# Kernel optimization log

Measured on AMD Instinct MI355X. Metric: run time of the kernel, lower is better.

The kernel has to match this reference:

```python
import jax, jax.numpy as jnp
import numpy as np

N_NODES = 50000
N_EDGES = 800000
BATCH = 4
D = 64


def setup_inputs() -> dict:
    key = jax.random.key(0)
    ks = jax.random.split(key, 8)
    state = jax.random.normal(ks[0], (BATCH, N_NODES, D), dtype=jnp.float32)
    edge_row = jax.random.randint(ks[1], (N_EDGES,), 0, N_NODES, dtype=jnp.int32)
    edge_col = jax.random.randint(ks[2], (N_EDGES,), 0, N_NODES, dtype=jnp.int32)
    edge_weight = jax.random.uniform(ks[3], (N_EDGES,), dtype=jnp.float32)
    stdv = 1.0 / np.sqrt(D)
    W1 = jax.random.uniform(ks[4], (D, D), minval=-stdv, maxval=stdv, dtype=jnp.float32)
    b1 = jnp.zeros((D,), dtype=jnp.float32)
    W2 = jax.random.uniform(ks[5], (D, D), minval=-stdv, maxval=stdv, dtype=jnp.float32)
    b2 = jnp.zeros((D,), dtype=jnp.float32)
    w_out = jax.random.normal(ks[6], (D,), dtype=jnp.float32) * stdv
    return {"state": state, "edge_row": edge_row, "edge_col": edge_col,
            "edge_weight": edge_weight, "W1": W1, "b1": b1, "W2": W2,
            "b2": b2, "w_out": w_out}


def _gcn_layer(x, W, bias, edge_row, edge_col, edge_weight, n, b):
    # x: [n, b, d_in] -> support [n, b, d_out]
    support = jnp.einsum('nbk,kp->nbp', x, W) + bias
    flat = support.reshape(n, -1)  # [n, b*d_out]
    # sparse spmm: out[i] = sum_{e: row_e=i} w_e * flat[col_e]
    msgs = edge_weight[:, None] * flat[edge_col]  # [E, b*d_out]
    out = jax.ops.segment_sum(msgs, edge_row, num_segments=n)
    return jax.nn.relu(out.reshape(n, b, -1))


def reference(state, edge_row, edge_col, edge_weight, W1, b1, W2, b2, w_out):
    b, n, _ = state.shape
    x = jnp.transpose(state, (1, 0, 2))  # [n, b, d]
    for W, bias in ((W1, b1), (W2, b2)):
        x = _gcn_layer(x, W, bias, edge_row, edge_col, edge_weight, n, b)
    # actor head: Linear(d,1,bias=False), squeeze, transpose -> [b, n]
    logits = jnp.einsum('nbd,d->nb', x, w_out)
    return logits.T
```

## Files before the change

### kernel.cpp

```cpp
#include <hip/hip_runtime.h>


typedef _Float16 fp16_t;
typedef _Float16 h4 __attribute__((ext_vector_type(4)));
typedef _Float16 h8 __attribute__((ext_vector_type(8)));
typedef float    f4 __attribute__((ext_vector_type(4)));
typedef unsigned long long ull;

#define CAP   64
#define RPB   256
#define BCAP  4608
#define CHK   3200
#define LROW  264
#define S1Q   (127.f / 4.f)
#define S1D   (4.f / 127.f)

__global__ __launch_bounds__(64) void prepW_k(const float* __restrict__ W,
                                              const float* __restrict__ bias,
                                              fp16_t* __restrict__ wf,
                                              float* __restrict__ bf,
                                              int* __restrict__ gcnt, int NB) {
    int lane = threadIdx.x;
    for (int i = lane; i < NB; i += 64) gcnt[i] = 0;
    int r16 = lane & 15, half = lane >> 4;
#pragma unroll
    for (int kk = 0; kk < 2; ++kk)
#pragma unroll
        for (int j = 0; j < 4; ++j) {
            h8 v;
#pragma unroll
            for (int t = 0; t < 8; ++t)
                v[t] = (_Float16)W[(32 * kk + 8 * half + t) * 64 + 16 * j + r16];
            *(h8*)&wf[((kk * 4 + j) * 64 + lane) * 8] = v;
        }
#pragma unroll
    for (int j = 0; j < 4; ++j) bf[j * 64 + lane] = bias[16 * j + r16];
}

__global__ __launch_bounds__(256) void bg_k(const int* __restrict__ erow,
                                            const int* __restrict__ ecol,
                                            const float* __restrict__ ew,
                                            int* __restrict__ gcnt,
                                            ull* __restrict__ bed,
                                            int E, int NB, int NB1,
                                            const float* __restrict__ xf,
                                            const float* __restrict__ W,
                                            const float* __restrict__ bias,
                                            unsigned char* __restrict__ flat1,
                                            int N) {
    if ((int)blockIdx.x < NB1) {
        __shared__ int hist[256], offs[256], cur[256], gbase[256];
        __shared__ ull stage[CHK];
        __shared__ unsigned short sbkt[CHK];
        int tid = threadIdx.x;
        int e0 = blockIdx.x * CHK;
        int e1 = e0 + CHK < E ? e0 + CHK : E;

        hist[tid] = 0;
        cur[tid] = 0;
        __syncthreads();
        for (int e = e0 + tid; e < e1; e += 256)
            atomicAdd(&hist[erow[e] >> 8], 1);
        __syncthreads();
        int v = hist[tid];
        offs[tid] = v;
        __syncthreads();
        for (int off = 1; off < 256; off <<= 1) {
            int t = (tid >= off) ? offs[tid - off] : 0;
            __syncthreads();
            offs[tid] += t;
            __syncthreads();
        }
        offs[tid] -= v;
        if (tid < NB && v > 0) gbase[tid] = atomicAdd(&gcnt[tid], v);
        __syncthreads();
        for (int e = e0 + tid; e < e1; e += 256) {
            int r = erow[e];
            int bk = r >> 8;
            unsigned q = (unsigned)(ew[e] * 32767.f + 0.5f);
            ull pv = ((ull)(r & 255) << 32) | (q << 17) | (unsigned)ecol[e];
            int idx = offs[bk] + atomicAdd(&cur[bk], 1);
            stage[idx] = pv;
            sbkt[idx] = (unsigned short)bk;
        }
        __syncthreads();
        int total = e1 - e0;
        for (int i = tid; i < total; i += 256) {
            int bk = sbkt[i];
            int sl = gbase[bk] + (i - offs[bk]);
            if (sl < BCAP) bed[(size_t)bk * BCAP + sl] = stage[i];
        }
    } else {
        int wave = threadIdx.x >> 6;
        int lane = threadIdx.x & 63;
        int r16 = lane & 15, half = lane >> 4;

        h8 Bf[2][4];
#pragma unroll
        for (int kk = 0; kk < 2; ++kk)
#pragma unroll
            for (int j = 0; j < 4; ++j) {
                h8 v;
#pragma unroll
                for (int t = 0; t < 8; ++t)
                    v[t] = (_Float16)W[(32 * kk + 8 * half + t) * 64 + 16 * j + r16];
                Bf[kk][j] = v;
            }
        float bj[4];
#pragma unroll
        for (int j = 0; j < 4; ++j) bj[j] = bias[16 * j + r16];

        int ntile = N >> 4;
        int gstride = gridDim.x - NB1;
        for (int tile = blockIdx.x - NB1; tile < ntile; tile += gstride) {
            int row = tile * 16 + r16;
            const float* p = xf + ((size_t)wave * N + row) * 64 + 8 * half;
            f4 u0 = *(const f4*)p;
            f4 u1 = *(const f4*)(p + 4);
            f4 u2 = *(const f4*)(p + 32);
            f4 u3 = *(const f4*)(p + 36);
            h8 A0, A1;
#pragma unroll
            for (int t = 0; t < 4; ++t) {
                A0[t] = (_Float16)u0[t]; A0[t + 4] = (_Float16)u1[t];
                A1[t] = (_Float16)u2[t]; A1[t + 4] = (_Float16)u3[t];
            }
#pragma unroll
            for (int j = 0; j < 4; ++j) {
                f4 c = {0.f, 0.f, 0.f, 0.f};
                c = __builtin_amdgcn_mfma_f32_16x16x32_f16(A0, Bf[0][j], c, 0, 0, 0);
                c = __builtin_amdgcn_mfma_f32_16x16x32_f16(A1, Bf[1][j], c, 0, 0, 0);
#pragma unroll
                for (int r = 0; r < 4; ++r) {
                    int orow = tile * 16 + 4 * half + r;
                    float fu = fmaf(c[r] + bj[j], S1Q, 128.f);
                    fu = fminf(fmaxf(fu, 0.f), 255.f);
                    flat1[(size_t)orow * 256 + wave * 64 + 16 * j + r16] =
                        (unsigned char)(fu + 0.5f);
                }
            }
        }
    }
}

__global__ __launch_bounds__(256) void build2_k(const ull* __restrict__ bed,
                                                const int* __restrict__ gcnt,
                                                unsigned* __restrict__ ed,
                                                int* __restrict__ cnt, int N) {
    __shared__ unsigned sbuf[RPB * CAP];
    __shared__ int scnt[RPB];
    int b = blockIdx.x, tid = threadIdx.x;
    for (int i = tid; i < RPB * CAP; i += 256) sbuf[i] = 0;
    scnt[tid] = 0;
    __syncthreads();
    int n = gcnt[b];
    n = n < BCAP ? n : BCAP;
    const ull* p = bed + (size_t)b * BCAP;
    for (int i = tid; i < n; i += 256) {
        ull v = p[i];
        int rl = (int)(v >> 32);
        int pos = atomicAdd(&scnt[rl], 1);
        if (pos < CAP) sbuf[(rl << 6) + pos] = (unsigned)v;
    }
    __syncthreads();
    size_t base = (size_t)b * (RPB * CAP);
    for (int i = tid; i < RPB * CAP; i += 256)
        ed[base + i] = sbuf[i];
    int r = b * RPB + tid;
    if (r < N) cnt[r] = scnt[tid] < CAP ? scnt[tid] : CAP;
}

#define EDGE4I(pk, A0, A1, A2, A3, WS)                                         \
    {                                                                          \
        unsigned _p = (pk);                                                    \
        float _w = (float)(_p >> 17) * (1.f / 32767.f);                        \
        unsigned _v = *(const unsigned*)(fb + ((size_t)(_p & 0x1FFFFu) << 8)   \
                                         + lane4);                             \
        A0 += _w * (float)(_v & 0xffu);                                        \
        A1 += _w * (float)((_v >> 8) & 0xffu);                                 \
        A2 += _w * (float)((_v >> 16) & 0xffu);                                \
        A3 += _w * (float)(_v >> 24);                                          \
        WS += _w;                                                              \
    }

__global__ __launch_bounds__(256) void spmmG_k(const unsigned char* __restrict__ flat,
                                               const int* __restrict__ cnt,
                                               const unsigned* __restrict__ ed,
                                               const fp16_t* __restrict__ wf,
                                               const float* __restrict__ bf,
                                               unsigned char* __restrict__ flat2i,
                                               float* __restrict__ s2, int N) {
    __shared__ fp16_t sagg[16 * LROW];
    __shared__ h8     swf[8 * 64];
    __shared__ float  sbf[4 * 64];
    int tid  = threadIdx.x;
    int wave = tid >> 6;
    int lane = tid & 63;
    int lane4 = lane * 4;
    int r16 = lane & 15, half = lane >> 4;

    ((f4*)swf)[tid] = ((const f4*)wf)[tid];
    ((f4*)swf)[tid + 256] = ((const f4*)wf)[tid + 256];
    sbf[tid] = bf[tid];

    int blk0 = blockIdx.x * 16;
    const char* fb = (const char*)flat;

#pragma unroll
    for (int pr = 0; pr < 2; ++pr) {
        int lr0 = wave * 4 + 2 * pr;
        int r0 = blk0 + lr0, r1 = r0 + 1;
        int m0 = __builtin_amdgcn_readfirstlane(cnt[r0]);
        int m1 = __builtin_amdgcn_readfirstlane(cnt[r1]);
        int mm = m0 > m1 ? m0 : m1;
        int mr = (mm + 3) & ~3;
        const unsigned* e0 = ed + (size_t)r0 * CAP;
        const unsigned* e1 = ed + (size_t)r1 * CAP;
        float a0 = 0.f, a1 = 0.f, a2 = 0.f, a3 = 0.f, wsA = 0.f;
        float c0 = 0.f, c1 = 0.f, c2 = 0.f, c3 = 0.f, wsC = 0.f;
        for (int j = 0; j < mr; j += 4) {
            uint4 pA = *(const uint4*)(e0 + j);
            uint4 pB = *(const uint4*)(e1 + j);
            EDGE4I(pA.x, a0, a1, a2, a3, wsA) EDGE4I(pB.x, c0, c1, c2, c3, wsC)
            EDGE4I(pA.y, a0, a1, a2, a3, wsA) EDGE4I(pB.y, c0, c1, c2, c3, wsC)
            EDGE4I(pA.z, a0, a1, a2, a3, wsA) EDGE4I(pB.z, c0, c1, c2, c3, wsC)
            EDGE4I(pA.w, a0, a1, a2, a3, wsA) EDGE4I(pB.w, c0, c1, c2, c3, wsC)
        }
        float bA = 128.f * wsA, bC = 128.f * wsC;
        h4 s0, s1;
        s0.x = (fp16_t)fmaxf(S1D * (a0 - bA), 0.f);
        s0.y = (fp16_t)fmaxf(S1D * (a1 - bA), 0.f);
        s0.z = (fp16_t)fmaxf(S1D * (a2 - bA), 0.f);
        s0.w = (fp16_t)fmaxf(S1D * (a3 - bA), 0.f);
        s1.x = (fp16_t)fmaxf(S1D * (c0 - bC), 0.f);
        s1.y = (fp16_t)fmaxf(S1D * (c1 - bC), 0.f);
        s1.z = (fp16_t)fmaxf(S1D * (c2 - bC), 0.f);
        s1.w = (fp16_t)fmaxf(S1D * (c3 - bC), 0.f);
        *(h4*)&sagg[lr0 * LROW + lane4] = s0;
        *(h4*)&sagg[(lr0 + 1) * LROW + lane4] = s1;
    }
    __syncthreads();

    h8 A0 = *(const h8*)&sagg[r16 * LROW + wave * 64 + 8 * half];
    h8 A1 = *(const h8*)&sagg[r16 * LROW + wave * 64 + 32 + 8 * half];
    f4 cc[4];
#pragma unroll
    for (int j = 0; j < 4; ++j) {
        f4 c = {0.f, 0.f, 0.f, 0.f};
        c = __builtin_amdgcn_mfma_f32_16x16x32_f16(A0, swf[j * 64 + lane], c, 0, 0, 0);
        c = __builtin_amdgcn_mfma_f32_16x16x32_f16(A1, swf[(4 + j) * 64 + lane], c, 0, 0, 0);
        float bjv = sbf[j * 64 + lane];
        c.x += bjv; c.y += bjv; c.z += bjv; c.w += bjv;
        cc[j] = c;
    }
#pragma unroll
    for (int r = 0; r < 4; ++r) {
        float m = fmaxf(fmaxf(fabsf(cc[0][r]), fabsf(cc[1][r])),
                        fmaxf(fabsf(cc[2][r]), fabsf(cc[3][r])));
        m = fmaxf(m, __shfl_xor(m, 1));
        m = fmaxf(m, __shfl_xor(m, 2));
        m = fmaxf(m, __shfl_xor(m, 4));
        m = fmaxf(m, __shfl_xor(m, 8));
        int orow = blk0 + 4 * half + r;
        float inv = (m > 0.f) ? (127.f / m) : 0.f;
        if (r16 == 0) s2[(orow << 2) | wave] = m * (1.f / 127.f);
#pragma unroll
        for (int j = 0; j < 4; ++j) {
            float q = fmaf(cc[j][r], inv, 128.f);
            flat2i[(size_t)orow * 256 + wave * 64 + 16 * j + r16] =
                (unsigned char)(q + 0.5f);
        }
    }
}

#define EDGE4Q(pk, A0, A1, A2, A3, WS)                                         \
    {                                                                          \
        unsigned _p = (pk);                                                    \
        unsigned _c = _p & 0x1FFFFu;                                           \
        float _w = (float)(_p >> 17) * (1.f / 32767.f) * s2[(_c << 2) | bsel]; \
        unsigned _v = *(const unsigned*)(fb + ((size_t)_c << 8) + lane4);      \
        A0 += _w * (float)(_v & 0xffu);                                        \
        A1 += _w * (float)((_v >> 8) & 0xffu);                                 \
        A2 += _w * (float)((_v >> 16) & 0xffu);                                \
        A3 += _w * (float)(_v >> 24);                                          \
        WS += _w;                                                              \
    }

__global__ __launch_bounds__(256) void spmm2h_k(const unsigned char* __restrict__ flat,
                                                const int* __restrict__ cnt,
                                                const unsigned* __restrict__ ed,
                                                const float* __restrict__ s2,
                                                const float* __restrict__ wout,
                                                float* __restrict__ out, int N) {
    int rowi = blockIdx.x * 4 + (int)(threadIdx.x >> 6);
    int lane = threadIdx.x & 63;
    int lane4 = lane * 4;
    int bsel = lane >> 4;
    const char* fb = (const char*)flat;
    int m = __builtin_amdgcn_readfirstlane(cnt[rowi]);
    int mr = (m + 7) & ~7;
    const unsigned* ep = ed + (size_t)rowi * CAP;
    float a0 = 0.f, a1 = 0.f, a2 = 0.f, a3 = 0.f, ws = 0.f;
    for (int j = 0; j < mr; j += 8) {
        uint4 pA = *(const uint4*)(ep + j);
        uint4 pB = *(const uint4*)(ep + j + 4);
        EDGE4Q(pA.x, a0, a1, a2, a3, ws) EDGE4Q(pA.y, a0, a1, a2, a3, ws)
        EDGE4Q(pA.z, a0, a1, a2, a3, ws) EDGE4Q(pA.w, a0, a1, a2, a3, ws)
        EDGE4Q(pB.x, a0, a1, a2, a3, ws) EDGE4Q(pB.y, a0, a1, a2, a3, ws)
        EDGE4Q(pB.z, a0, a1, a2, a3, ws) EDGE4Q(pB.w, a0, a1, a2, a3, ws)
    }
    float bs = 128.f * ws;
    int t = lane & 15;
    float4 wo = ((const float4*)wout)[t];
    float p = fmaxf(a0 - bs, 0.f) * wo.x + fmaxf(a1 - bs, 0.f) * wo.y +
              fmaxf(a2 - bs, 0.f) * wo.z + fmaxf(a3 - bs, 0.f) * wo.w;
    p += __shfl_xor(p, 1); p += __shfl_xor(p, 2);
    p += __shfl_xor(p, 4); p += __shfl_xor(p, 8);
    if (t == 0) out[(size_t)bsel * N + rowi] = p;
}

extern "C" void kernel_launch(void* const* d_in, const int* in_sizes, int n_in,
                              void* d_out, int out_size, void* d_ws, size_t ws_size,
                              hipStream_t stream) {
    const float* state = (const float*)d_in[0];
    const int*   erow  = (const int*)d_in[1];
    const int*   ecol  = (const int*)d_in[2];
    const float* ew    = (const float*)d_in[3];
    const float* W1    = (const float*)d_in[4];
    const float* b1    = (const float*)d_in[5];
    const float* W2    = (const float*)d_in[6];
    const float* b2    = (const float*)d_in[7];
    const float* wout  = (const float*)d_in[8];
    float* out = (float*)d_out;

    int N = in_sizes[0] / (4 * 64);
    int E = in_sizes[1];
    int NB = (N + RPB - 1) / RPB;

    char* ws = (char*)d_ws;
    size_t off = 0;
    auto alloc = [&](size_t bytes) -> char* {
        char* p = ws + off;
        off += (bytes + 255) & ~(size_t)255;
        return p;
    };
    unsigned char* flat1  = (unsigned char*)alloc((size_t)N * 256);
    unsigned char* flat2i = (unsigned char*)alloc((size_t)N * 256);
    float*    s2    = (float*)alloc((size_t)N * 4 * 4);
    int*      cnt   = (int*)alloc((size_t)NB * RPB * 4);
    unsigned* ed    = (unsigned*)alloc((size_t)NB * RPB * CAP * 4);
    int*      gcnt  = (int*)alloc((size_t)NB * 4);
    ull*      bed   = (ull*)alloc((size_t)NB * BCAP * 8);
    fp16_t*   wf    = (fp16_t*)alloc(8 * 64 * 8 * 2);
    float*    bfr   = (float*)alloc(4 * 64 * 4);
    if (off > ws_size) return;

    prepW_k<<<1, 64, 0, stream>>>(W2, b2, wf, bfr, gcnt, NB);
    int nblk1 = (E + CHK - 1) / CHK;
    bg_k<<<nblk1 + 1024, 256, 0, stream>>>(erow, ecol, ew, gcnt, bed, E, NB,
                                           nblk1, state, W1, b1, flat1, N);
    build2_k<<<NB, 256, 0, stream>>>(bed, gcnt, ed, cnt, N);
    spmmG_k<<<N / 16, 256, 0, stream>>>(flat1, cnt, ed, wf, bfr, flat2i, s2, N);
    spmm2h_k<<<(N + 3) / 4, 256, 0, stream>>>(flat2i, cnt, ed, s2, wout, out, N);
}
```

Baseline: 112.2 us.

## Regroup kernels so layer-1 GEMM overlaps bucket build and pair rows by degree

The weight-prep work moves into the edge-bucketing kernel, and the gcnt zeroing becomes a memset. The layer-1 dense GEMM now runs inside the second-stage bucket-to-row builder (1024-thread blocks) rather than alongside the first bucketing pass. In the SpMM, each wave now picks the pairing of its four rows that minimises padded loop trips, so rows with similar degree share a loop. This rebalances which independent work overlaps and cuts divergence waste, at the cost of larger blocks with heavy LDS use in the builder and a changed launch shape for the GEMM.

```diff
diff --git a/kernel.cpp b/kernel.cpp
--- a/kernel.cpp
+++ b/kernel.cpp
@@ -15,84 +15,113 @@
 #define S1Q   (127.f / 4.f)
 #define S1D   (4.f / 127.f)
 
-__global__ __launch_bounds__(64) void prepW_k(const float* __restrict__ W,
+__global__ __launch_bounds__(256) void b1p_k(const int* __restrict__ erow,
+                                             const int* __restrict__ ecol,
+                                             const float* __restrict__ ew,
+                                             int* __restrict__ gcnt,
+                                             ull* __restrict__ bed,
+                                             int E, int NB, int NB1,
+                                             const float* __restrict__ W,
+                                             const float* __restrict__ bias,
+                                             fp16_t* __restrict__ wf,
+                                             float* __restrict__ bf) {
+    if ((int)blockIdx.x == NB1) {
+        int lane = threadIdx.x;
+        if (lane < 64) {
+            int r16 = lane & 15, half = lane >> 4;
+#pragma unroll
+            for (int kk = 0; kk < 2; ++kk)
+#pragma unroll
+                for (int j = 0; j < 4; ++j) {
+                    h8 v;
+#pragma unroll
+                    for (int t = 0; t < 8; ++t)
+                        v[t] = (_Float16)W[(32 * kk + 8 * half + t) * 64 + 16 * j + r16];
+                    *(h8*)&wf[((kk * 4 + j) * 64 + lane) * 8] = v;
+                }
+#pragma unroll
+            for (int j = 0; j < 4; ++j) bf[j * 64 + lane] = bias[16 * j + r16];
+        }
+        return;
+    }
+    __shared__ int hist[256], offs[256], cur[256], gbase[256];
+    __shared__ ull stage[CHK];
+    __shared__ unsigned short sbkt[CHK];
+    int tid = threadIdx.x;
+    int e0 = blockIdx.x * CHK;
+    int e1 = e0 + CHK < E ? e0 + CHK : E;
+
+    hist[tid] = 0;
+    cur[tid] = 0;
+    __syncthreads();
+    for (int e = e0 + tid; e < e1; e += 256)
+        atomicAdd(&hist[erow[e] >> 8], 1);
+    __syncthreads();
+    int v = hist[tid];
+    offs[tid] = v;
+    __syncthreads();
+    for (int off = 1; off < 256; off <<= 1) {
+        int t = (tid >= off) ? offs[tid - off] : 0;
+        __syncthreads();
+        offs[tid] += t;
+        __syncthreads();
+    }
+    offs[tid] -= v;
+    if (tid < NB && v > 0) gbase[tid] = atomicAdd(&gcnt[tid], v);
+    __syncthreads();
+    for (int e = e0 + tid; e < e1; e += 256) {
+        int r = erow[e];
+        int bk = r >> 8;
+        unsigned q = (unsigned)(ew[e] * 32767.f + 0.5f);
+        ull pv = ((ull)(r & 255) << 32) | (q << 17) | (unsigned)ecol[e];
+        int idx = offs[bk] + atomicAdd(&cur[bk], 1);
+        stage[idx] = pv;
+        sbkt[idx] = (unsigned short)bk;
+    }
+    __syncthreads();
+    int total = e1 - e0;
+    for (int i = tid; i < total; i += 256) {
+        int bk = sbkt[i];
+        int sl = gbase[bk] + (i - offs[bk]);
+        if (sl < BCAP) bed[(size_t)bk * BCAP + sl] = stage[i];
+    }
+}
+
+__global__ __launch_bounds__(1024) void bg2_k(const ull* __restrict__ bed,
+                                              const int* __restrict__ gcnt,
+                                              unsigned* __restrict__ ed,
+                                              int* __restrict__ cnt,
+                                              int N, int NB,
+                                              const float* __restrict__ xf,
+                                              const float* __restrict__ W,
                                               const float* __restrict__ bias,
-                                              fp16_t* __restrict__ wf,
-                                              float* __restrict__ bf,
-                                              int* __restrict__ gcnt, int NB) {
-    int lane = threadIdx.x;
-    for (int i = lane; i < NB; i += 64) gcnt[i] = 0;
-    int r16 = lane & 15, half = lane >> 4;
-#pragma unroll
-    for (int kk = 0; kk < 2; ++kk)
-#pragma unroll
-        for (int j = 0; j < 4; ++j) {
-            h8 v;
-#pragma unroll
-            for (int t = 0; t < 8; ++t)
-                v[t] = (_Float16)W[(32 * kk + 8 * half + t) * 64 + 16 * j + r16];
-            *(h8*)&wf[((kk * 4 + j) * 64 + lane) * 8] = v;
-        }
-#pragma unroll
-    for (int j = 0; j < 4; ++j) bf[j * 64 + lane] = bias[16 * j + r16];
-}
-
-__global__ __launch_bounds__(256) void bg_k(const int* __restrict__ erow,
-                                            const int* __restrict__ ecol,
-                                            const float* __restrict__ ew,
-                                            int* __restrict__ gcnt,
-                                            ull* __restrict__ bed,
-                                            int E, int NB, int NB1,
-                                            const float* __restrict__ xf,
-                                            const float* __restrict__ W,
-                                            const float* __restrict__ bias,
-                                            unsigned char* __restrict__ flat1,
-                                            int N) {
-    if ((int)blockIdx.x < NB1) {
-        __shared__ int hist[256], offs[256], cur[256], gbase[256];
-        __shared__ ull stage[CHK];
-        __shared__ unsigned short sbkt[CHK];
+                                              unsigned char* __restrict__ flat1) {
+    if ((int)blockIdx.x < NB) {
+        __shared__ unsigned sbuf[RPB * CAP];
+        __shared__ int scnt[RPB];
+        int b = blockIdx.x, tid = threadIdx.x;
+        for (int i = tid; i < RPB * CAP; i += 1024) sbuf[i] = 0;
+        if (tid < RPB) scnt[tid] = 0;
+        __syncthreads();
+        int n = gcnt[b];
+        n = n < BCAP ? n : BCAP;
+        const ull* p = bed + (size_t)b * BCAP;
+        for (int i = tid; i < n; i += 1024) {
+            ull v = p[i];
+            int rl = (int)(v >> 32);
+            int pos = atomicAdd(&scnt[rl], 1);
+            if (pos < CAP) sbuf[(rl << 6) + pos] = (unsigned)v;
+        }
+        __syncthreads();
+        size_t base = (size_t)b * (RPB * CAP);
+        for (int i = tid; i < RPB * CAP; i += 1024)
+            ed[base + i] = sbuf[i];
+        int r = b * RPB + tid;
+        if (tid < RPB && r < N) cnt[r] = scnt[tid] < CAP ? scnt[tid] : CAP;
+    } else {
         int tid = threadIdx.x;
-        int e0 = blockIdx.x * CHK;
-        int e1 = e0 + CHK < E ? e0 + CHK : E;
-
-        hist[tid] = 0;
-        cur[tid] = 0;
-        __syncthreads();
-        for (int e = e0 + tid; e < e1; e += 256)
-            atomicAdd(&hist[erow[e] >> 8], 1);
-        __syncthreads();
-        int v = hist[tid];
-        offs[tid] = v;
-        __syncthreads();
-        for (int off = 1; off < 256; off <<= 1) {
-            int t = (tid >= off) ? offs[tid - off] : 0;
-            __syncthreads();
-            offs[tid] += t;
-            __syncthreads();
-        }
-        offs[tid] -= v;
-        if (tid < NB && v > 0) gbase[tid] = atomicAdd(&gcnt[tid], v);
-        __syncthreads();
-        for (int e = e0 + tid; e < e1; e += 256) {
-            int r = erow[e];
-            int bk = r >> 8;
-            unsigned q = (unsigned)(ew[e] * 32767.f + 0.5f);
-            ull pv = ((ull)(r & 255) << 32) | (q << 17) | (unsigned)ecol[e];
-            int idx = offs[bk] + atomicAdd(&cur[bk], 1);
-            stage[idx] = pv;
-            sbkt[idx] = (unsigned short)bk;
-        }
-        __syncthreads();
-        int total = e1 - e0;
-        for (int i = tid; i < total; i += 256) {
-            int bk = sbkt[i];
-            int sl = gbase[bk] + (i - offs[bk]);
-            if (sl < BCAP) bed[(size_t)bk * BCAP + sl] = stage[i];
-        }
-    } else {
-        int wave = threadIdx.x >> 6;
-        int lane = threadIdx.x & 63;
+        int wave = tid >> 6, lane = tid & 63;
+        int batch = wave & 3, tsub = wave >> 2;
         int r16 = lane & 15, half = lane >> 4;
 
         h8 Bf[2][4];
@@ -111,10 +140,11 @@
         for (int j = 0; j < 4; ++j) bj[j] = bias[16 * j + r16];
 
         int ntile = N >> 4;
-        int gstride = gridDim.x - NB1;
-        for (int tile = blockIdx.x - NB1; tile < ntile; tile += gstride) {
+        int gstride = ((int)gridDim.x - NB) * 4;
+        for (int tile = ((int)blockIdx.x - NB) * 4 + tsub; tile < ntile;
+             tile += gstride) {
             int row = tile * 16 + r16;
-            const float* p = xf + ((size_t)wave * N + row) * 64 + 8 * half;
+            const float* p = xf + ((size_t)batch * N + row) * 64 + 8 * half;
             f4 u0 = *(const f4*)p;
             f4 u1 = *(const f4*)(p + 4);
             f4 u2 = *(const f4*)(p + 32);
@@ -135,39 +165,12 @@
                     int orow = tile * 16 + 4 * half + r;
                     float fu = fmaf(c[r] + bj[j], S1Q, 128.f);
                     fu = fminf(fmaxf(fu, 0.f), 255.f);
-                    flat1[(size_t)orow * 256 + wave * 64 + 16 * j + r16] =
+                    flat1[(size_t)orow * 256 + batch * 64 + 16 * j + r16] =
                         (unsigned char)(fu + 0.5f);
                 }
             }
         }
     }
-}
-
-__global__ __launch_bounds__(256) void build2_k(const ull* __restrict__ bed,
-                                                const int* __restrict__ gcnt,
-                                                unsigned* __restrict__ ed,
-                                                int* __restrict__ cnt, int N) {
-    __shared__ unsigned sbuf[RPB * CAP];
-    __shared__ int scnt[RPB];
-    int b = blockIdx.x, tid = threadIdx.x;
-    for (int i = tid; i < RPB * CAP; i += 256) sbuf[i] = 0;
-    scnt[tid] = 0;
-    __syncthreads();
-    int n = gcnt[b];
-    n = n < BCAP ? n : BCAP;
-    const ull* p = bed + (size_t)b * BCAP;
-    for (int i = tid; i < n; i += 256) {
-        ull v = p[i];
-        int rl = (int)(v >> 32);
-        int pos = atomicAdd(&scnt[rl], 1);
-        if (pos < CAP) sbuf[(rl << 6) + pos] = (unsigned)v;
-    }
-    __syncthreads();
-    size_t base = (size_t)b * (RPB * CAP);
-    for (int i = tid; i < RPB * CAP; i += 256)
-        ed[base + i] = sbuf[i];
-    int r = b * RPB + tid;
-    if (r < N) cnt[r] = scnt[tid] < CAP ? scnt[tid] : CAP;
 }
 
 #define EDGE4I(pk, A0, A1, A2, A3, WS)                                         \
@@ -205,17 +208,29 @@
 
     int blk0 = blockIdx.x * 16;
     const char* fb = (const char*)flat;
-
+    int r0 = blk0 + wave * 4;
+
+    int mm0 = __builtin_amdgcn_readfirstlane(cnt[r0]);
+    int mm1 = __builtin_amdgcn_readfirstlane(cnt[r0 + 1]);
+    int mm2 = __builtin_amdgcn_readfirstlane(cnt[r0 + 2]);
+    int mm3 = __builtin_amdgcn_readfirstlane(cnt[r0 + 3]);
+#define C4(a, b) ((((a) > (b) ? (a) : (b)) + 3) & ~3)
+    int cA = C4(mm0, mm1) + C4(mm2, mm3);
+    int cB = C4(mm0, mm2) + C4(mm1, mm3);
+    int cC = C4(mm0, mm3) + C4(mm1, mm2);
+    int i1, i2, i3, mI1, mI2, mI3;
+    if (cA <= cB && cA <= cC) { i1 = 1; i2 = 2; i3 = 3; mI1 = mm1; mI2 = mm2; mI3 = mm3; }
+    else if (cB <= cC)        { i1 = 2; i2 = 1; i3 = 3; mI1 = mm2; mI2 = mm1; mI3 = mm3; }
+    else                      { i1 = 3; i2 = 1; i3 = 2; mI1 = mm3; mI2 = mm1; mI3 = mm2; }
+
+    int pa[2] = {0, i2}, pb[2] = {i1, i3};
+    int pma[2] = {mm0, mI2}, pmb[2] = {mI1, mI3};
 #pragma unroll
     for (int pr = 0; pr < 2; ++pr) {
-        int lr0 = wave * 4 + 2 * pr;
-        int r0 = blk0 + lr0, r1 = r0 + 1;
-        int m0 = __builtin_amdgcn_readfirstlane(cnt[r0]);
-        int m1 = __builtin_amdgcn_readfirstlane(cnt[r1]);
-        int mm = m0 > m1 ? m0 : m1;
-        int mr = (mm + 3) & ~3;
-        const unsigned* e0 = ed + (size_t)r0 * CAP;
-        const unsigned* e1 = ed + (size_t)r1 * CAP;
+        int la = pa[pr], lb = pb[pr];
+        int mr = C4(pma[pr], pmb[pr]);
+        const unsigned* e0 = ed + (size_t)(r0 + la) * CAP;
+        const unsigned* e1 = ed + (size_t)(r0 + lb) * CAP;
         float a0 = 0.f, a1 = 0.f, a2 = 0.f, a3 = 0.f, wsA = 0.f;
         float c0 = 0.f, c1 = 0.f, c2 = 0.f, c3 = 0.f, wsC = 0.f;
         for (int j = 0; j < mr; j += 4) {
@@ -236,9 +251,10 @@
         s1.y = (fp16_t)fmaxf(S1D * (c1 - bC), 0.f);
         s1.z = (fp16_t)fmaxf(S1D * (c2 - bC), 0.f);
         s1.w = (fp16_t)fmaxf(S1D * (c3 - bC), 0.f);
-        *(h4*)&sagg[lr0 * LROW + lane4] = s0;
-        *(h4*)&sagg[(lr0 + 1) * LROW + lane4] = s1;
-    }
+        *(h4*)&sagg[(wave * 4 + la) * LROW + lane4] = s0;
+        *(h4*)&sagg[(wave * 4 + lb) * LROW + lane4] = s1;
+    }
+#undef C4
     __syncthreads();
 
     h8 A0 = *(const h8*)&sagg[r16 * LROW + wave * 64 + 8 * half];
@@ -355,11 +371,12 @@
     float*    bfr   = (float*)alloc(4 * 64 * 4);
     if (off > ws_size) return;
 
-    prepW_k<<<1, 64, 0, stream>>>(W2, b2, wf, bfr, gcnt, NB);
     int nblk1 = (E + CHK - 1) / CHK;
-    bg_k<<<nblk1 + 1024, 256, 0, stream>>>(erow, ecol, ew, gcnt, bed, E, NB,
-                                           nblk1, state, W1, b1, flat1, N);
-    build2_k<<<NB, 256, 0, stream>>>(bed, gcnt, ed, cnt, N);
+    hipMemsetAsync(gcnt, 0, (size_t)NB * 4, stream);
+    b1p_k<<<nblk1 + 1, 256, 0, stream>>>(erow, ecol, ew, gcnt, bed, E, NB,
+                                         nblk1, W2, b2, wf, bfr);
+    bg2_k<<<NB + 256, 1024, 0, stream>>>(bed, gcnt, ed, cnt, N, NB,
+                                         state, W1, b1, flat1);
     spmmG_k<<<N / 16, 256, 0, stream>>>(flat1, cnt, ed, wf, bfr, flat2i, s2, N);
     spmm2h_k<<<(N + 3) / 4, 256, 0, stream>>>(flat2i, cnt, ed, s2, wout, out, N);
 }
```

Result: no change. 114.1 us (+1.7%).
